# Optimization experiments

Measured on AMD Instinct MI355X. Metric: run time of the kernel, lower is better.

The kernel has to match this reference:

```python
import jax, jax.numpy as jnp
import numpy as np
import math

N_EMBD = 1024
N_HEAD = 16
BLOCK = 2048
B, T = 2, 2048


def setup_inputs() -> dict:
    key = jax.random.key(0)
    ks = jax.random.split(key, 5)
    s = 0.02
    return {
        "x": jax.random.normal(ks[0], (B, T, N_EMBD), dtype=jnp.float32),
        "W_attn": jax.random.normal(ks[1], (3 * N_EMBD, N_EMBD), dtype=jnp.float32) * s,  # [out,in] torch layout
        "b_attn": jax.random.normal(ks[2], (3 * N_EMBD,), dtype=jnp.float32) * s,
        "W_proj": jax.random.normal(ks[3], (N_EMBD, N_EMBD), dtype=jnp.float32) * s,
        "b_proj": jax.random.normal(ks[4], (N_EMBD,), dtype=jnp.float32) * s,
    }


def reference(x, W_attn, b_attn, W_proj, b_proj):
    Bx, Tx, C = x.shape
    H = N_HEAD
    D = C // H
    qkv = jnp.einsum("btc,oc->bto", x, W_attn) + b_attn  # [B,T,3C]
    q, k, v = jnp.split(qkv, 3, axis=-1)
    # [B,T,H,D] -> [B,H,T,D]
    q = q.reshape(Bx, Tx, H, D).transpose(0, 2, 1, 3)
    k = k.reshape(Bx, Tx, H, D).transpose(0, 2, 1, 3)
    v = v.reshape(Bx, Tx, H, D).transpose(0, 2, 1, 3)
    att = jnp.einsum("bhqd,bhkd->bhqk", q, k) * (1.0 / math.sqrt(D))
    causal = jnp.tril(jnp.ones((Tx, Tx), dtype=bool))
    att = jnp.where(causal[None, None], att, -jnp.inf)
    att = jax.nn.softmax(att, axis=-1)
    y = jnp.einsum("bhqk,bhkd->bhqd", att, v)  # [B,H,T,D]
    y = y.transpose(0, 2, 1, 3).reshape(Bx, Tx, C)
    y = jnp.einsum("btc,oc->bto", y, W_proj) + b_proj
    return y
```

## Files before the change

### kernel.cpp

```cpp
#include <hip/hip_runtime.h>
#include <hip/hip_bf16.h>
#include <stdint.h>

typedef unsigned short u16;
using f32x4 = __attribute__((ext_vector_type(4))) float;
using s16x8 = __attribute__((ext_vector_type(8))) short;

#define B_SZ 2
#define T_SZ 2048
#define C_SZ 1024
#define H_SZ 16
#define D_SZ 64

#define Q_SCALE 0.18033688011112042f

__device__ __forceinline__ u16 f2bf(float f) {
  __hip_bfloat16 h = __float2bfloat16(f);
  return *(u16*)&h;
}

__device__ __forceinline__ void async16(const u16* g, u16* l) {
  __builtin_amdgcn_global_load_lds((__attribute__((address_space(1))) void*)(g),
                                   (__attribute__((address_space(3))) void*)(l),
                                   16, 0, 0);
}

__global__ void cvt3_kernel(const float* __restrict__ a, int na,
                            const float* __restrict__ b, int nb,
                            const float* __restrict__ c, int nc,
                            u16* __restrict__ out) {
  int n = na + nb + nc;
  for (int i = blockIdx.x * blockDim.x + threadIdx.x; i < n; i += gridDim.x * blockDim.x) {
    const float* src; int off;
    if (i < na)           { src = a; off = i; }
    else if (i < na + nb) { src = b; off = i - na; }
    else                  { src = c; off = i - na - nb; }
    float4 v = reinterpret_cast<const float4*>(src)[off];
    ushort4 o;
    o.x = f2bf(v.x); o.y = f2bf(v.y); o.z = f2bf(v.z); o.w = f2bf(v.w);
    reinterpret_cast<ushort4*>(out)[i] = o;
  }
}

__global__ __launch_bounds__(256) void gemm_qkv(
    const u16* __restrict__ A, const u16* __restrict__ W,
    const float* __restrict__ bias,
    u16* __restrict__ Qo, u16* __restrict__ Ko, u16* __restrict__ Vt)
{
  const int K = 1024;
  const int NT = 32;
  __shared__ __align__(16) u16 lA[2][128 * 32];
  __shared__ __align__(16) u16 lB[2][128 * 32];
  int tid = threadIdx.x, lane = tid & 63, wave = tid >> 6;
  int wm = (wave >> 1) * 64, wn = (wave & 1) * 64;
  int bm = blockIdx.x * 128, bn = blockIdx.y * 128;
  int r = lane & 15, g = lane >> 4;

  int p0 = tid, p1 = 256 + tid;
  int ar0 = p0 >> 2, ar1 = p1 >> 2;
  int al0 = (p0 & 3) ^ (ar0 & 3), al1 = (p1 & 3) ^ (ar1 & 3);
  const u16* As0 = A + (size_t)(bm + ar0) * K + al0 * 8;
  const u16* As1 = A + (size_t)(bm + ar1) * K + al1 * 8;
  const u16* Ws0 = W + (size_t)(bn + ar0) * K + al0 * 8;
  const u16* Ws1 = W + (size_t)(bn + ar1) * K + al1 * 8;

  f32x4 acc[4][4];
#pragma unroll
  for (int i = 0; i < 4; ++i)
#pragma unroll
    for (int j = 0; j < 4; ++j)
      acc[i][j] = (f32x4){0.f, 0.f, 0.f, 0.f};

  int rd_off = r * 32 + ((g ^ (r & 3)) * 8);

  async16(As0, &lA[0][p0 * 8]);
  async16(As1, &lA[0][p1 * 8]);
  async16(Ws0, &lB[0][p0 * 8]);
  async16(Ws1, &lB[0][p1 * 8]);
  __syncthreads();

  int cur = 0;
  for (int t = 0; t < NT; ++t) {
    if (t + 1 < NT) {
      int k0 = (t + 1) * 32;
      int nb_ = cur ^ 1;
      async16(As0 + k0, &lA[nb_][p0 * 8]);
      async16(As1 + k0, &lA[nb_][p1 * 8]);
      async16(Ws0 + k0, &lB[nb_][p0 * 8]);
      async16(Ws1 + k0, &lB[nb_][p1 * 8]);
    }
    s16x8 af[4], bf[4];
#pragma unroll
    for (int i = 0; i < 4; ++i)
      af[i] = *(const s16x8*)(&lA[cur][(wm + i * 16) * 32 + rd_off]);
#pragma unroll
    for (int j = 0; j < 4; ++j)
      bf[j] = *(const s16x8*)(&lB[cur][(wn + j * 16) * 32 + rd_off]);
#pragma unroll
    for (int i = 0; i < 4; ++i)
#pragma unroll
      for (int j = 0; j < 4; ++j)
        acc[i][j] = __builtin_amdgcn_mfma_f32_16x16x32_bf16(af[i], bf[j], acc[i][j], 0, 0, 0);
    __syncthreads();
    cur ^= 1;
  }

  int seg = bn >> 10;
#pragma unroll
  for (int i = 0; i < 4; ++i) {
#pragma unroll
    for (int j = 0; j < 4; ++j) {
      int col = bn + wn + j * 16 + r;
      int cc = col & 1023;
      int h = cc >> 6, d = cc & 63;
      float bv = bias[col];
      int row0 = bm + wm + i * 16 + g * 4;
      int b = row0 >> 11, t0 = row0 & 2047;
      if (seg == 2) {
        ushort4 pv;
        pv.x = f2bf(acc[i][j][0] + bv);
        pv.y = f2bf(acc[i][j][1] + bv);
        pv.z = f2bf(acc[i][j][2] + bv);
        pv.w = f2bf(acc[i][j][3] + bv);
        *reinterpret_cast<ushort4*>(Vt + ((size_t)(b * H_SZ + h) * D_SZ + d) * T_SZ + t0) = pv;
      } else {
        u16* dst = (seg == 0) ? Qo : Ko;
        float scale = (seg == 0) ? Q_SCALE : 1.0f;
#pragma unroll
        for (int rr = 0; rr < 4; ++rr) {
          float v = (acc[i][j][rr] + bv) * scale;
          dst[(((size_t)(b * H_SZ + h) * T_SZ + (t0 + rr)) * D_SZ) + d] = f2bf(v);
        }
      }
    }
  }
}

__global__ __launch_bounds__(256) void gemm_proj(
    const u16* __restrict__ A, const u16* __restrict__ W,
    const float* __restrict__ bias, float* __restrict__ out)
{
  const int K = 1024;
  const int NT = 32;
  __shared__ __align__(16) u16 lA[2][128 * 32];
  __shared__ __align__(16) u16 lB[2][128 * 32];
  int tid = threadIdx.x, lane = tid & 63, wave = tid >> 6;
  int wm = (wave >> 1) * 64, wn = (wave & 1) * 64;
  int bm = blockIdx.x * 128, bn = blockIdx.y * 128;
  int r = lane & 15, g = lane >> 4;

  int p0 = tid, p1 = 256 + tid;
  int ar0 = p0 >> 2, ar1 = p1 >> 2;
  int al0 = (p0 & 3) ^ (ar0 & 3), al1 = (p1 & 3) ^ (ar1 & 3);
  const u16* As0 = A + (size_t)(bm + ar0) * K + al0 * 8;
  const u16* As1 = A + (size_t)(bm + ar1) * K + al1 * 8;
  const u16* Ws0 = W + (size_t)(bn + ar0) * K + al0 * 8;
  const u16* Ws1 = W + (size_t)(bn + ar1) * K + al1 * 8;

  f32x4 acc[4][4];
#pragma unroll
  for (int i = 0; i < 4; ++i)
#pragma unroll
    for (int j = 0; j < 4; ++j)
      acc[i][j] = (f32x4){0.f, 0.f, 0.f, 0.f};

  int rd_off = r * 32 + ((g ^ (r & 3)) * 8);

  async16(As0, &lA[0][p0 * 8]);
  async16(As1, &lA[0][p1 * 8]);
  async16(Ws0, &lB[0][p0 * 8]);
  async16(Ws1, &lB[0][p1 * 8]);
  __syncthreads();

  int cur = 0;
  for (int t = 0; t < NT; ++t) {
    if (t + 1 < NT) {
      int k0 = (t + 1) * 32;
      int nb_ = cur ^ 1;
      async16(As0 + k0, &lA[nb_][p0 * 8]);
      async16(As1 + k0, &lA[nb_][p1 * 8]);
      async16(Ws0 + k0, &lB[nb_][p0 * 8]);
      async16(Ws1 + k0, &lB[nb_][p1 * 8]);
    }
    s16x8 af[4], bf[4];
#pragma unroll
    for (int i = 0; i < 4; ++i)
      af[i] = *(const s16x8*)(&lA[cur][(wm + i * 16) * 32 + rd_off]);
#pragma unroll
    for (int j = 0; j < 4; ++j)
      bf[j] = *(const s16x8*)(&lB[cur][(wn + j * 16) * 32 + rd_off]);
#pragma unroll
    for (int i = 0; i < 4; ++i)
#pragma unroll
      for (int j = 0; j < 4; ++j)
        acc[i][j] = __builtin_amdgcn_mfma_f32_16x16x32_bf16(af[i], bf[j], acc[i][j], 0, 0, 0);
    __syncthreads();
    cur ^= 1;
  }

#pragma unroll
  for (int i = 0; i < 4; ++i) {
#pragma unroll
    for (int j = 0; j < 4; ++j) {
      int col = bn + wn + j * 16 + r;
      float bv = bias[col];
#pragma unroll
      for (int rr = 0; rr < 4; ++rr) {
        int row = bm + wm + i * 16 + g * 4 + rr;
        out[(size_t)row * 1024 + col] = acc[i][j][rr] + bv;
      }
    }
  }
}

__global__ __launch_bounds__(256) void attn_kernel(
    const u16* __restrict__ Q, const u16* __restrict__ K, const u16* __restrict__ Vt,
    u16* __restrict__ Y)
{
  __shared__ __align__(16) u16 lK[2][64 * 64];
  __shared__ __align__(16) u16 lV[2][64 * 64];
  __shared__ __align__(16) u16 lP[4][16 * 64];
  int tid = threadIdx.x, lane = tid & 63, wave = tid >> 6;
  int bh = blockIdx.x;
  int qt = 31 - blockIdx.y;
  const u16* Qh = Q + (size_t)bh * T_SZ * D_SZ;
  const u16* Kh = K + (size_t)bh * T_SZ * D_SZ;
  const u16* Vh = Vt + (size_t)bh * D_SZ * T_SZ;
  int r = lane & 15, g = lane >> 4;
  int wq = qt * 64 + wave * 16;
  int qrow = wq + r;

  s16x8 qf0 = *(const s16x8*)(Qh + (size_t)qrow * 64 + g * 8);
  s16x8 qf1 = *(const s16x8*)(Qh + (size_t)qrow * 64 + 32 + g * 8);

  int p0 = tid, p1 = 256 + tid;
  int r0 = p0 >> 3, r1 = p1 >> 3;
  int l0 = (p0 & 7) ^ (r0 & 7), l1 = (p1 & 7) ^ (r1 & 7);

  float m = -3e30f, s = 0.f;
  f32x4 o[4];
#pragma unroll
  for (int j = 0; j < 4; ++j) o[j] = (f32x4){0.f, 0.f, 0.f, 0.f};

  u16* lPw = lP[wave];

  async16(Kh + (size_t)r0 * 64 + l0 * 8, &lK[0][p0 * 8]);
  async16(Kh + (size_t)r1 * 64 + l1 * 8, &lK[0][p1 * 8]);
  async16(Vh + (size_t)r0 * T_SZ + l0 * 8, &lV[0][p0 * 8]);
  async16(Vh + (size_t)r1 * T_SZ + l1 * 8, &lV[0][p1 * 8]);
  __syncthreads();

  int cur = 0;
  for (int kt = 0; kt <= qt; ++kt) {
    int kvbase = kt * 64;
    if (kt < qt) {
      int nb_ = cur ^ 1;
      int kb = kvbase + 64;
      async16(Kh + (size_t)(kb + r0) * 64 + l0 * 8, &lK[nb_][p0 * 8]);
      async16(Kh + (size_t)(kb + r1) * 64 + l1 * 8, &lK[nb_][p1 * 8]);
      async16(Vh + (size_t)r0 * T_SZ + kb + l0 * 8, &lV[nb_][p0 * 8]);
      async16(Vh + (size_t)r1 * T_SZ + kb + l1 * 8, &lV[nb_][p1 * 8]);
    }

    f32x4 sf[4];
    __builtin_amdgcn_s_setprio(1);
#pragma unroll
    for (int jj = 0; jj < 4; ++jj) {
      int krow = jj * 16 + r;
      const s16x8 kf0 = *(const s16x8*)(&lK[cur][krow * 64 + ((g ^ (r & 7)) * 8)]);
      const s16x8 kf1 = *(const s16x8*)(&lK[cur][krow * 64 + (((4 + g) ^ (r & 7)) * 8)]);
      f32x4 sv = (f32x4){0.f, 0.f, 0.f, 0.f};
      sv = __builtin_amdgcn_mfma_f32_16x16x32_bf16(kf0, qf0, sv, 0, 0, 0);
      sv = __builtin_amdgcn_mfma_f32_16x16x32_bf16(kf1, qf1, sv, 0, 0, 0);
      sf[jj] = sv;
    }
    __builtin_amdgcn_s_setprio(0);

    float mx = -3e30f;
    if (kt == qt) {
#pragma unroll
      for (int jj = 0; jj < 4; ++jj)
#pragma unroll
        for (int rr = 0; rr < 4; ++rr) {
          int kv = kvbase + jj * 16 + g * 4 + rr;
          float v = (kv <= qrow) ? sf[jj][rr] : -3e30f;
          sf[jj][rr] = v;
          mx = fmaxf(mx, v);
        }
    } else {
#pragma unroll
      for (int jj = 0; jj < 4; ++jj)
#pragma unroll
        for (int rr = 0; rr < 4; ++rr) mx = fmaxf(mx, sf[jj][rr]);
    }
    mx = fmaxf(mx, __shfl_xor(mx, 16));
    mx = fmaxf(mx, __shfl_xor(mx, 32));

    float corr = 1.0f;
    if (!__all(mx <= m + 8.0f)) {
      float mnew = fmaxf(m, mx);
      corr = __builtin_amdgcn_exp2f(m - mnew);
      m = mnew;
#pragma unroll
      for (int j = 0; j < 4; ++j)
#pragma unroll
        for (int rr = 0; rr < 4; ++rr) o[j][rr] *= corr;
    }

    float rsum = 0.f;
#pragma unroll
    for (int jj = 0; jj < 4; ++jj)
#pragma unroll
      for (int rr = 0; rr < 4; ++rr) {
        float p = __builtin_amdgcn_exp2f(sf[jj][rr] - m);
        sf[jj][rr] = p;
        rsum += p;
      }
    rsum += __shfl_xor(rsum, 16);
    rsum += __shfl_xor(rsum, 32);
    s = s * corr + rsum;

#pragma unroll
    for (int jj = 0; jj < 4; ++jj) {
      ushort4 pk;
      pk.x = f2bf(sf[jj][0]); pk.y = f2bf(sf[jj][1]);
      pk.z = f2bf(sf[jj][2]); pk.w = f2bf(sf[jj][3]);
      int off = r * 64 + ((jj * 16 + 4 * g) ^ ((r & 7) << 3));
      *reinterpret_cast<ushort4*>(lPw + off) = pk;
    }

    __builtin_amdgcn_s_setprio(1);
#pragma unroll
    for (int hh = 0; hh < 2; ++hh) {
      const s16x8 pa = *(const s16x8*)(lPw + r * 64 + (((hh * 4 + g) ^ (r & 7)) * 8));
#pragma unroll
      for (int j = 0; j < 4; ++j) {
        int vrow = j * 16 + r;
        const s16x8 vb = *(const s16x8*)(&lV[cur][vrow * 64 + (((hh * 4 + g) ^ (r & 7)) * 8)]);
        o[j] = __builtin_amdgcn_mfma_f32_16x16x32_bf16(vb, pa, o[j], 0, 0, 0);
      }
    }
    __builtin_amdgcn_s_setprio(0);
    __syncthreads();
    cur ^= 1;
  }

  float sinv = 1.0f / s;
  int b = bh >> 4, h = bh & 15;
  size_t ybase = ((size_t)(b * T_SZ + qrow)) * C_SZ + h * 64;
#pragma unroll
  for (int j = 0; j < 4; ++j) {
    ushort4 pk;
    pk.x = f2bf(o[j][0] * sinv);
    pk.y = f2bf(o[j][1] * sinv);
    pk.z = f2bf(o[j][2] * sinv);
    pk.w = f2bf(o[j][3] * sinv);
    *reinterpret_cast<ushort4*>(Y + ybase + j * 16 + g * 4) = pk;
  }
}

extern "C" void kernel_launch(void* const* d_in, const int* in_sizes, int n_in,
                              void* d_out, int out_size, void* d_ws, size_t ws_size,
                              hipStream_t stream) {
  const float* x      = (const float*)d_in[0];
  const float* W_attn = (const float*)d_in[1];
  const float* b_attn = (const float*)d_in[2];
  const float* W_proj = (const float*)d_in[3];
  const float* b_proj = (const float*)d_in[4];
  float* out = (float*)d_out;

  char* ws = (char*)d_ws;
  u16* xb  = (u16*)ws; ws += (size_t)4096 * 1024 * 2;
  u16* wab = (u16*)ws; ws += (size_t)3072 * 1024 * 2;
  u16* wpb = (u16*)ws; ws += (size_t)1024 * 1024 * 2;
  u16* Qb  = (u16*)ws; ws += (size_t)B_SZ * H_SZ * T_SZ * D_SZ * 2;
  u16* Kb  = (u16*)ws; ws += (size_t)B_SZ * H_SZ * T_SZ * D_SZ * 2;
  u16* Vtb = (u16*)ws; ws += (size_t)B_SZ * H_SZ * T_SZ * D_SZ * 2;
  u16* Yb  = (u16*)ws; ws += (size_t)4096 * 1024 * 2;

  int n4x = 4096 * 1024 / 4;
  int n4a = 3072 * 1024 / 4;
  int n4p = 1024 * 1024 / 4;
  cvt3_kernel<<<2048, 256, 0, stream>>>(x, n4x, W_attn, n4a, W_proj, n4p, xb);

  gemm_qkv<<<dim3(32, 24), 256, 0, stream>>>(xb, wab, b_attn, Qb, Kb, Vtb);
  attn_kernel<<<dim3(32, 32), 256, 0, stream>>>(Qb, Kb, Vtb, Yb);
  gemm_proj<<<dim3(32, 8), 256, 0, stream>>>(Yb, wpb, b_proj, out);
}
```

Measured before the change: 119.2 us.

## Pair complementary causal query tiles per attention block for load balance

Each attention workgroup now processes two query tiles, qt=31-i and qt=i, so every block does the same total number of KV iterations and the grid halves to 512 blocks. This targets the tail imbalance of causal attention, where long and short tiles are scheduled unevenly. It also moves the row-sum shuffle reduction out of the inner loop to the end and skips the max shuffles when no rescale is needed. The cost is fewer blocks, which can lower occupancy on a large GPU, and serial execution of the two halves inside one block.

```diff
diff --git a/kernel.cpp b/kernel.cpp
--- a/kernel.cpp
+++ b/kernel.cpp
@@ -222,140 +222,143 @@
   __shared__ __align__(16) u16 lP[4][16 * 64];
   int tid = threadIdx.x, lane = tid & 63, wave = tid >> 6;
   int bh = blockIdx.x;
-  int qt = 31 - blockIdx.y;
+  int pairIdx = blockIdx.y;
   const u16* Qh = Q + (size_t)bh * T_SZ * D_SZ;
   const u16* Kh = K + (size_t)bh * T_SZ * D_SZ;
   const u16* Vh = Vt + (size_t)bh * D_SZ * T_SZ;
   int r = lane & 15, g = lane >> 4;
-  int wq = qt * 64 + wave * 16;
-  int qrow = wq + r;
-
-  s16x8 qf0 = *(const s16x8*)(Qh + (size_t)qrow * 64 + g * 8);
-  s16x8 qf1 = *(const s16x8*)(Qh + (size_t)qrow * 64 + 32 + g * 8);
 
   int p0 = tid, p1 = 256 + tid;
   int r0 = p0 >> 3, r1 = p1 >> 3;
   int l0 = (p0 & 7) ^ (r0 & 7), l1 = (p1 & 7) ^ (r1 & 7);
 
-  float m = -3e30f, s = 0.f;
-  f32x4 o[4];
-#pragma unroll
-  for (int j = 0; j < 4; ++j) o[j] = (f32x4){0.f, 0.f, 0.f, 0.f};
-
   u16* lPw = lP[wave];
-
-  async16(Kh + (size_t)r0 * 64 + l0 * 8, &lK[0][p0 * 8]);
-  async16(Kh + (size_t)r1 * 64 + l1 * 8, &lK[0][p1 * 8]);
-  async16(Vh + (size_t)r0 * T_SZ + l0 * 8, &lV[0][p0 * 8]);
-  async16(Vh + (size_t)r1 * T_SZ + l1 * 8, &lV[0][p1 * 8]);
-  __syncthreads();
-
+  int b = bh >> 4, h = bh & 15;
   int cur = 0;
-  for (int kt = 0; kt <= qt; ++kt) {
-    int kvbase = kt * 64;
-    if (kt < qt) {
-      int nb_ = cur ^ 1;
-      int kb = kvbase + 64;
-      async16(Kh + (size_t)(kb + r0) * 64 + l0 * 8, &lK[nb_][p0 * 8]);
-      async16(Kh + (size_t)(kb + r1) * 64 + l1 * 8, &lK[nb_][p1 * 8]);
-      async16(Vh + (size_t)r0 * T_SZ + kb + l0 * 8, &lV[nb_][p0 * 8]);
-      async16(Vh + (size_t)r1 * T_SZ + kb + l1 * 8, &lV[nb_][p1 * 8]);
-    }
-
-    f32x4 sf[4];
-    __builtin_amdgcn_s_setprio(1);
-#pragma unroll
-    for (int jj = 0; jj < 4; ++jj) {
-      int krow = jj * 16 + r;
-      const s16x8 kf0 = *(const s16x8*)(&lK[cur][krow * 64 + ((g ^ (r & 7)) * 8)]);
-      const s16x8 kf1 = *(const s16x8*)(&lK[cur][krow * 64 + (((4 + g) ^ (r & 7)) * 8)]);
-      f32x4 sv = (f32x4){0.f, 0.f, 0.f, 0.f};
-      sv = __builtin_amdgcn_mfma_f32_16x16x32_bf16(kf0, qf0, sv, 0, 0, 0);
-      sv = __builtin_amdgcn_mfma_f32_16x16x32_bf16(kf1, qf1, sv, 0, 0, 0);
-      sf[jj] = sv;
-    }
-    __builtin_amdgcn_s_setprio(0);
-
-    float mx = -3e30f;
-    if (kt == qt) {
+
+  for (int phase = 0; phase < 2; ++phase) {
+    int qt = phase == 0 ? (31 - pairIdx) : pairIdx;
+    int wq = qt * 64 + wave * 16;
+    int qrow = wq + r;
+
+    s16x8 qf0 = *(const s16x8*)(Qh + (size_t)qrow * 64 + g * 8);
+    s16x8 qf1 = *(const s16x8*)(Qh + (size_t)qrow * 64 + 32 + g * 8);
+
+    float m = -3e30f, s = 0.f;
+    f32x4 o[4];
+#pragma unroll
+    for (int j = 0; j < 4; ++j) o[j] = (f32x4){0.f, 0.f, 0.f, 0.f};
+
+    async16(Kh + (size_t)r0 * 64 + l0 * 8, &lK[cur][p0 * 8]);
+    async16(Kh + (size_t)r1 * 64 + l1 * 8, &lK[cur][p1 * 8]);
+    async16(Vh + (size_t)r0 * T_SZ + l0 * 8, &lV[cur][p0 * 8]);
+    async16(Vh + (size_t)r1 * T_SZ + l1 * 8, &lV[cur][p1 * 8]);
+    __syncthreads();
+
+    for (int kt = 0; kt <= qt; ++kt) {
+      int kvbase = kt * 64;
+      if (kt < qt) {
+        int nb_ = cur ^ 1;
+        int kb = kvbase + 64;
+        async16(Kh + (size_t)(kb + r0) * 64 + l0 * 8, &lK[nb_][p0 * 8]);
+        async16(Kh + (size_t)(kb + r1) * 64 + l1 * 8, &lK[nb_][p1 * 8]);
+        async16(Vh + (size_t)r0 * T_SZ + kb + l0 * 8, &lV[nb_][p0 * 8]);
+        async16(Vh + (size_t)r1 * T_SZ + kb + l1 * 8, &lV[nb_][p1 * 8]);
+      }
+
+      f32x4 sf[4];
+      __builtin_amdgcn_s_setprio(1);
+#pragma unroll
+      for (int jj = 0; jj < 4; ++jj) {
+        int krow = jj * 16 + r;
+        const s16x8 kf0 = *(const s16x8*)(&lK[cur][krow * 64 + ((g ^ (r & 7)) * 8)]);
+        const s16x8 kf1 = *(const s16x8*)(&lK[cur][krow * 64 + (((4 + g) ^ (r & 7)) * 8)]);
+        f32x4 sv = (f32x4){0.f, 0.f, 0.f, 0.f};
+        sv = __builtin_amdgcn_mfma_f32_16x16x32_bf16(kf0, qf0, sv, 0, 0, 0);
+        sv = __builtin_amdgcn_mfma_f32_16x16x32_bf16(kf1, qf1, sv, 0, 0, 0);
+        sf[jj] = sv;
+      }
+      __builtin_amdgcn_s_setprio(0);
+
+      float mxp = -3e30f;
+      if (kt == qt) {
+#pragma unroll
+        for (int jj = 0; jj < 4; ++jj)
+#pragma unroll
+          for (int rr = 0; rr < 4; ++rr) {
+            int kv = kvbase + jj * 16 + g * 4 + rr;
+            float v = (kv <= qrow) ? sf[jj][rr] : -3e30f;
+            sf[jj][rr] = v;
+            mxp = fmaxf(mxp, v);
+          }
+      } else {
+#pragma unroll
+        for (int jj = 0; jj < 4; ++jj)
+#pragma unroll
+          for (int rr = 0; rr < 4; ++rr) mxp = fmaxf(mxp, sf[jj][rr]);
+      }
+
+      if (!__all(mxp <= m + 8.0f)) {
+        float mx = fmaxf(mxp, __shfl_xor(mxp, 16));
+        mx = fmaxf(mx, __shfl_xor(mx, 32));
+        float mnew = fmaxf(m, mx);
+        float corr = __builtin_amdgcn_exp2f(m - mnew);
+        m = mnew;
+        s *= corr;
+#pragma unroll
+        for (int j = 0; j < 4; ++j)
+#pragma unroll
+          for (int rr = 0; rr < 4; ++rr) o[j][rr] *= corr;
+      }
+
 #pragma unroll
       for (int jj = 0; jj < 4; ++jj)
 #pragma unroll
         for (int rr = 0; rr < 4; ++rr) {
-          int kv = kvbase + jj * 16 + g * 4 + rr;
-          float v = (kv <= qrow) ? sf[jj][rr] : -3e30f;
-          sf[jj][rr] = v;
-          mx = fmaxf(mx, v);
+          float p = __builtin_amdgcn_exp2f(sf[jj][rr] - m);
+          sf[jj][rr] = p;
+          s += p;
         }
-    } else {
-#pragma unroll
-      for (int jj = 0; jj < 4; ++jj)
-#pragma unroll
-        for (int rr = 0; rr < 4; ++rr) mx = fmaxf(mx, sf[jj][rr]);
-    }
-    mx = fmaxf(mx, __shfl_xor(mx, 16));
-    mx = fmaxf(mx, __shfl_xor(mx, 32));
-
-    float corr = 1.0f;
-    if (!__all(mx <= m + 8.0f)) {
-      float mnew = fmaxf(m, mx);
-      corr = __builtin_amdgcn_exp2f(m - mnew);
-      m = mnew;
-#pragma unroll
-      for (int j = 0; j < 4; ++j)
-#pragma unroll
-        for (int rr = 0; rr < 4; ++rr) o[j][rr] *= corr;
-    }
-
-    float rsum = 0.f;
-#pragma unroll
-    for (int jj = 0; jj < 4; ++jj)
-#pragma unroll
-      for (int rr = 0; rr < 4; ++rr) {
-        float p = __builtin_amdgcn_exp2f(sf[jj][rr] - m);
-        sf[jj][rr] = p;
-        rsum += p;
-      }
-    rsum += __shfl_xor(rsum, 16);
-    rsum += __shfl_xor(rsum, 32);
-    s = s * corr + rsum;
-
-#pragma unroll
-    for (int jj = 0; jj < 4; ++jj) {
+
+#pragma unroll
+      for (int jj = 0; jj < 4; ++jj) {
+        ushort4 pk;
+        pk.x = f2bf(sf[jj][0]); pk.y = f2bf(sf[jj][1]);
+        pk.z = f2bf(sf[jj][2]); pk.w = f2bf(sf[jj][3]);
+        int off = r * 64 + ((jj * 16 + 4 * g) ^ ((r & 7) << 3));
+        *reinterpret_cast<ushort4*>(lPw + off) = pk;
+      }
+
+      __builtin_amdgcn_s_setprio(1);
+#pragma unroll
+      for (int hh = 0; hh < 2; ++hh) {
+        const s16x8 pa = *(const s16x8*)(lPw + r * 64 + (((hh * 4 + g) ^ (r & 7)) * 8));
+#pragma unroll
+        for (int j = 0; j < 4; ++j) {
+          int vrow = j * 16 + r;
+          const s16x8 vb = *(const s16x8*)(&lV[cur][vrow * 64 + (((hh * 4 + g) ^ (r & 7)) * 8)]);
+          o[j] = __builtin_amdgcn_mfma_f32_16x16x32_bf16(vb, pa, o[j], 0, 0, 0);
+        }
+      }
+      __builtin_amdgcn_s_setprio(0);
+      __syncthreads();
+      cur ^= 1;
+    }
+
+    float sfull = s;
+    sfull += __shfl_xor(sfull, 16);
+    sfull += __shfl_xor(sfull, 32);
+    float sinv = 1.0f / sfull;
+    size_t ybase = ((size_t)(b * T_SZ + qrow)) * C_SZ + h * 64;
+#pragma unroll
+    for (int j = 0; j < 4; ++j) {
       ushort4 pk;
-      pk.x = f2bf(sf[jj][0]); pk.y = f2bf(sf[jj][1]);
-      pk.z = f2bf(sf[jj][2]); pk.w = f2bf(sf[jj][3]);
-      int off = r * 64 + ((jj * 16 + 4 * g) ^ ((r & 7) << 3));
-      *reinterpret_cast<ushort4*>(lPw + off) = pk;
-    }
-
-    __builtin_amdgcn_s_setprio(1);
-#pragma unroll
-    for (int hh = 0; hh < 2; ++hh) {
-      const s16x8 pa = *(const s16x8*)(lPw + r * 64 + (((hh * 4 + g) ^ (r & 7)) * 8));
-#pragma unroll
-      for (int j = 0; j < 4; ++j) {
-        int vrow = j * 16 + r;
-        const s16x8 vb = *(const s16x8*)(&lV[cur][vrow * 64 + (((hh * 4 + g) ^ (r & 7)) * 8)]);
-        o[j] = __builtin_amdgcn_mfma_f32_16x16x32_bf16(vb, pa, o[j], 0, 0, 0);
-      }
-    }
-    __builtin_amdgcn_s_setprio(0);
-    __syncthreads();
-    cur ^= 1;
-  }
-
-  float sinv = 1.0f / s;
-  int b = bh >> 4, h = bh & 15;
-  size_t ybase = ((size_t)(b * T_SZ + qrow)) * C_SZ + h * 64;
-#pragma unroll
-  for (int j = 0; j < 4; ++j) {
-    ushort4 pk;
-    pk.x = f2bf(o[j][0] * sinv);
-    pk.y = f2bf(o[j][1] * sinv);
-    pk.z = f2bf(o[j][2] * sinv);
-    pk.w = f2bf(o[j][3] * sinv);
-    *reinterpret_cast<ushort4*>(Y + ybase + j * 16 + g * 4) = pk;
+      pk.x = f2bf(o[j][0] * sinv);
+      pk.y = f2bf(o[j][1] * sinv);
+      pk.z = f2bf(o[j][2] * sinv);
+      pk.w = f2bf(o[j][3] * sinv);
+      *reinterpret_cast<ushort4*>(Y + ybase + j * 16 + g * 4) = pk;
+    }
   }
 }
 
@@ -384,6 +387,6 @@
   cvt3_kernel<<<2048, 256, 0, stream>>>(x, n4x, W_attn, n4a, W_proj, n4p, xb);
 
   gemm_qkv<<<dim3(32, 24), 256, 0, stream>>>(xb, wab, b_attn, Qb, Kb, Vtb);
-  attn_kernel<<<dim3(32, 32), 256, 0, stream>>>(Qb, Kb, Vtb, Yb);
+  attn_kernel<<<dim3(32, 16), 256, 0, stream>>>(Qb, Kb, Vtb, Yb);
   gemm_proj<<<dim3(32, 8), 256, 0, stream>>>(Yb, wpb, b_proj, out);
 }
```

Result: no change. 116.9 us (-1.9%).
